# Kernel tuning notes

Hardware: AMD Instinct MI355X
Metric: run time of the kernel (lower is better)

## Reference

```python
import jax, jax.numpy as jnp
import numpy as np

MOL_SIZE = 64      # points per molecule (all molecules equal-size -> block-diagonal attn)
NUM_HEADS = 8
CUTOFF = 8.0
NUM_RBF = 32
LN_EPS = 1e-5


def setup_inputs() -> dict:
    key = jax.random.key(0)
    ks = jax.random.split(key, 6)
    B, K, hidden = 1024, MOL_SIZE, 512
    H = NUM_HEADS
    N = B * K
    h = jax.random.normal(ks[0], (N, hidden), jnp.float32)
    pos = jax.random.normal(ks[1], (N, 3), jnp.float32) * 3.0  # spread so dists hit RBF centers
    batch = jnp.repeat(jnp.arange(B, dtype=jnp.int32), K)
    s = lambda fin: 1.0 / np.sqrt(fin)
    centers = jnp.linspace(0.0, CUTOFF, NUM_RBF).astype(jnp.float32)  # RBFEncoder buffer
    w_rbf = jax.random.normal(ks[2], (NUM_RBF, H), jnp.float32) * s(NUM_RBF)
    b_rbf = jnp.zeros((H,), jnp.float32)
    w_qkv = jax.random.normal(ks[3], (hidden, 3 * hidden), jnp.float32) * s(hidden)
    b_qkv = jnp.zeros((3 * hidden,), jnp.float32)
    w_out = jax.random.normal(ks[4], (hidden, hidden), jnp.float32) * s(hidden)
    b_out = jnp.zeros((hidden,), jnp.float32)
    gamma = jnp.ones((hidden,), jnp.float32)
    beta = jnp.zeros((hidden,), jnp.float32)
    return {"h": h, "pos": pos, "batch": batch, "centers": centers,
            "w_rbf": w_rbf, "b_rbf": b_rbf, "w_qkv": w_qkv, "b_qkv": b_qkv,
            "w_out": w_out, "b_out": b_out, "gamma": gamma, "beta": beta}


def reference(h, pos, batch, centers, w_rbf, b_rbf, w_qkv, b_qkv, w_out, b_out, gamma, beta):
    N, hidden = h.shape
    K = MOL_SIZE
    B = N // K
    H = NUM_HEADS
    D = hidden // H
    width = (CUTOFF / NUM_RBF) ** 2
    scale = D ** -0.5

    # equal-size contiguous molecules -> reshape equals per-molecule loop
    hb = h.reshape(B, K, hidden)
    pb = pos.reshape(B, K, 3)

    qkv = hb @ w_qkv + b_qkv                      # [B,K,3*hidden]
    q, k, v = jnp.split(qkv, 3, axis=-1)
    q = q.reshape(B, K, H, D)
    k = k.reshape(B, K, H, D)
    v = v.reshape(B, K, H, D)

    diff = pb[:, :, None, :] - pb[:, None, :, :]  # [B,K,K,3]
    dist = jnp.sqrt(jnp.maximum(jnp.sum(diff * diff, axis=-1), 1e-12))  # torch.cdist
    rbf = jnp.exp(-((dist[..., None] - centers) ** 2) / width)          # [B,K,K,R]
    bias = jnp.transpose(rbf @ w_rbf + b_rbf, (0, 3, 1, 2))             # [B,H,K,K]

    attn = jnp.einsum('bkhd,bjhd->bhkj', q, k) * scale + bias
    attn = jax.nn.softmax(attn, axis=-1)
    agg = jnp.einsum('bhkj,bjhd->bkhd', attn, v).reshape(B, K, hidden)
    out = agg @ w_out + b_out

    y = hb + out
    mu = jnp.mean(y, axis=-1, keepdims=True)
    var = jnp.var(y, axis=-1, keepdims=True)
    y = (y - mu) / jnp.sqrt(var + LN_EPS) * gamma + beta
    return y.reshape(N, hidden)
```

## Files before the change

kernel.cpp:

```cpp
#include <hip/hip_runtime.h>
#include <hip/hip_bf16.h>


#define HID 512
#define TBL 2048
#define DMAX 12.0f

typedef __attribute__((ext_vector_type(4))) float f32x4;
typedef __attribute__((ext_vector_type(8))) short bhalf8;

__device__ __forceinline__ short f2bf(float f) {
    union { float f; unsigned u; } x; x.f = f;
    unsigned u = x.u;
    unsigned r = (u + 0x7FFFu + ((u >> 16) & 1u)) >> 16;
    return (short)r;
}

__global__ __launch_bounds__(256) void k_prep_w(const float* __restrict__ w_qkv,
                                                const float* __restrict__ w_out,
                                                short* __restrict__ wqT,
                                                short* __restrict__ woT) {
    __shared__ short tile[64][68];
    const int t = threadIdx.x;
    int bt = blockIdx.x;
    const float* src; short* dst; int sld, tk, tc;
    if (bt < 192) { src = w_qkv; dst = wqT; sld = 1536; tk = bt & 7; tc = bt >> 3; }
    else { int b2 = bt - 192; src = w_out; dst = woT; sld = 512; tk = b2 & 7; tc = b2 >> 3; }
#pragma unroll
    for (int p = 0; p < 4; ++p) {
        int s = t + 256 * p;
        int r = s >> 4, sg = s & 15;
        const float4 v = *(const float4*)(src + (tk * 64 + r) * sld + tc * 64 + sg * 4);
        tile[r][sg * 4 + 0] = f2bf(v.x);
        tile[r][sg * 4 + 1] = f2bf(v.y);
        tile[r][sg * 4 + 2] = f2bf(v.z);
        tile[r][sg * 4 + 3] = f2bf(v.w);
    }
    __syncthreads();
#pragma unroll
    for (int p = 0; p < 16; ++p) {
        int o = t + 256 * p;
        int c = o >> 6, k = o & 63;
        dst[(tc * 64 + c) * 512 + tk * 64 + k] = tile[k][c];
    }
}

__global__ __launch_bounds__(256) void k_prep_tbl(const float* __restrict__ centers,
                                                  const float* __restrict__ w_rbf,
                                                  const float* __restrict__ b_rbf,
                                                  float* __restrict__ tbl) {
    int idx = blockIdx.x * 256 + threadIdx.x;
    int hh = idx >> 11, i = idx & (TBL - 1);
    float d = (float)i * (DMAX / (float)(TBL - 1));
    float s = b_rbf[hh];
    const float invw = 1.0f / 0.0625f;
#pragma unroll 4
    for (int r = 0; r < 32; ++r) {
        float tt = d - centers[r];
        s += w_rbf[r * 8 + hh] * expf(-(tt * tt) * invw);
    }
    tbl[idx] = s;
}

__global__ __launch_bounds__(512) void k_qkv(const float* __restrict__ h,
                                             const float* __restrict__ b_qkv,
                                             const short* __restrict__ wqT,
                                             short* __restrict__ qkvb,
                                             int molbase) {
    __shared__ __align__(16) short As[128 * 40];
    __shared__ __align__(16) short Bs[256 * 40];
    const int t = threadIdx.x;
    const int lane = t & 63, wave = t >> 6;
    const int l16 = lane & 15, g = lane >> 4;
    const int wrow = wave >> 2, wcol = wave & 3;
    const int R0 = molbase * 64 + blockIdx.x * 128;
    const int C0 = blockIdx.y * 256;

    f32x4 acc[4][4];
#pragma unroll
    for (int i = 0; i < 4; ++i)
#pragma unroll
        for (int j = 0; j < 4; ++j) acc[i][j] = (f32x4){0.f, 0.f, 0.f, 0.f};

    const int arow = t >> 2, aseg = t & 3;
    for (int kc = 0; kc < 16; ++kc) {
        const int kb = kc * 32;
        {
            const float* src = h + (R0 + arow) * HID + kb + aseg * 8;
            float4 v0 = *(const float4*)src;
            float4 v1 = *(const float4*)(src + 4);
            short s8[8];
            s8[0] = f2bf(v0.x); s8[1] = f2bf(v0.y); s8[2] = f2bf(v0.z); s8[3] = f2bf(v0.w);
            s8[4] = f2bf(v1.x); s8[5] = f2bf(v1.y); s8[6] = f2bf(v1.z); s8[7] = f2bf(v1.w);
            *(int4*)(&As[arow * 40 + aseg * 8]) = *(int4*)s8;
        }
#pragma unroll
        for (int p = 0; p < 2; ++p) {
            int flat = p * 512 + t;
            int col = flat >> 2, seg = flat & 3;
            *(int4*)(&Bs[col * 40 + seg * 8]) =
                *(const int4*)(wqT + (C0 + col) * HID + kb + seg * 8);
        }
        __syncthreads();
        bhalf8 af[4], bf[4];
#pragma unroll
        for (int mt = 0; mt < 4; ++mt)
            af[mt] = *(const bhalf8*)(&As[(wrow * 64 + mt * 16 + l16) * 40 + g * 8]);
#pragma unroll
        for (int nt = 0; nt < 4; ++nt)
            bf[nt] = *(const bhalf8*)(&Bs[(wcol * 64 + nt * 16 + l16) * 40 + g * 8]);
#pragma unroll
        for (int mt = 0; mt < 4; ++mt)
#pragma unroll
            for (int nt = 0; nt < 4; ++nt)
                acc[mt][nt] = __builtin_amdgcn_mfma_f32_16x16x32_bf16(af[mt], bf[nt], acc[mt][nt], 0, 0, 0);
        __syncthreads();
    }

    const int sec = C0 >> 9;
    const float mul = (sec == 0) ? 0.125f : 1.0f;
#pragma unroll
    for (int nt = 0; nt < 4; ++nt) {
        int c = C0 + wcol * 64 + nt * 16 + l16;
        float bv = b_qkv[c];
        int head = (c >> 6) & 7, d = c & 63;
#pragma unroll
        for (int mt = 0; mt < 4; ++mt) {
            int rowg = R0 + wrow * 64 + mt * 16 + g * 4;
            int mol_local = (rowg >> 6) - molbase;
            short* panel = qkvb + (size_t)((mol_local * 3 + sec) * 8 + head) * 4096;
            int rloc = rowg & 63;
#pragma unroll
            for (int r = 0; r < 4; ++r)
                panel[(rloc + r) * 64 + d] = f2bf((acc[mt][nt][r] + bv) * mul);
        }
    }
}

__global__ __launch_bounds__(256) void k_attn(const short* __restrict__ qkvb,
                                              const float* __restrict__ pos,
                                              const float* __restrict__ tbl,
                                              float* __restrict__ agg,
                                              int molbase) {
    __shared__ __align__(16) short sq[64 * 72];
    __shared__ __align__(16) short sk[64 * 72];
    __shared__ __align__(16) short svT[64 * 72];
    __shared__ __align__(16) short sp[64 * 72];
    __shared__ float s_tbl[TBL];
    __shared__ float s_px[64], s_py[64], s_pz[64];

    const int bid = blockIdx.x;
    const int mol_local = bid >> 3, head = bid & 7;
    const int t = threadIdx.x;
    const int wave = t >> 6, lane = t & 63;
    const int l16 = lane & 15, g = lane >> 4;
    const int rowbase = (molbase + mol_local) * 64;

    const short* qp = qkvb + (size_t)((mol_local * 3 + 0) * 8 + head) * 4096;
    const short* kp = qkvb + (size_t)((mol_local * 3 + 1) * 8 + head) * 4096;
    const short* vp = qkvb + (size_t)((mol_local * 3 + 2) * 8 + head) * 4096;

#pragma unroll
    for (int p = 0; p < 2; ++p) {
        int slot = p * 256 + t;
        int row = slot >> 3, seg = slot & 7;
        *(int4*)(&sq[row * 72 + seg * 8]) = *(const int4*)(qp + slot * 8);
        *(int4*)(&sk[row * 72 + seg * 8]) = *(const int4*)(kp + slot * 8);
        int4 vv = *(const int4*)(vp + slot * 8);
        short* vs = (short*)&vv;
#pragma unroll
        for (int j = 0; j < 8; ++j) svT[(seg * 8 + j) * 72 + row] = vs[j];
    }
    for (int i = t; i < TBL; i += 256) s_tbl[i] = tbl[head * TBL + i];
    if (t < 64) {
        s_px[t] = pos[(rowbase + t) * 3 + 0];
        s_py[t] = pos[(rowbase + t) * 3 + 1];
        s_pz[t] = pos[(rowbase + t) * 3 + 2];
    }
    __syncthreads();

    f32x4 sacc[4];
#pragma unroll
    for (int i = 0; i < 4; ++i) sacc[i] = (f32x4){0.f, 0.f, 0.f, 0.f};
    const int srow = wave * 16 + l16;
#pragma unroll
    for (int kk = 0; kk < 2; ++kk) {
        bhalf8 a = *(const bhalf8*)(&sq[srow * 72 + kk * 32 + g * 8]);
#pragma unroll
        for (int ct = 0; ct < 4; ++ct) {
            bhalf8 b = *(const bhalf8*)(&sk[(ct * 16 + l16) * 72 + kk * 32 + g * 8]);
            sacc[ct] = __builtin_amdgcn_mfma_f32_16x16x32_bf16(a, b, sacc[ct], 0, 0, 0);
        }
    }

    const int r0 = wave * 16 + g * 4;
    const float tscale = (float)(TBL - 1) / DMAX;
#pragma unroll
    for (int ct = 0; ct < 4; ++ct) {
        int col = ct * 16 + l16;
        float cx = s_px[col], cy = s_py[col], cz = s_pz[col];
#pragma unroll
        for (int r = 0; r < 4; ++r) {
            int row = r0 + r;
            float dx = s_px[row] - cx, dy = s_py[row] - cy, dz = s_pz[row] - cz;
            float dd = fmaf(dx, dx, fmaf(dy, dy, dz * dz));
            float dist = sqrtf(fmaxf(dd, 1e-12f));
            float u = fminf(dist, DMAX) * tscale;
            int i = (int)u; if (i > TBL - 2) i = TBL - 2;
            float fr = u - (float)i;
            float t0 = s_tbl[i];
            sacc[ct][r] += fmaf(fr, s_tbl[i + 1] - t0, t0);
        }
    }

    float inv[4];
#pragma unroll
    for (int r = 0; r < 4; ++r) {
        float m = fmaxf(fmaxf(sacc[0][r], sacc[1][r]), fmaxf(sacc[2][r], sacc[3][r]));
#pragma unroll
        for (int off = 1; off < 16; off <<= 1) m = fmaxf(m, __shfl_xor(m, off, 64));
        float e0 = __expf(sacc[0][r] - m);
        float e1 = __expf(sacc[1][r] - m);
        float e2 = __expf(sacc[2][r] - m);
        float e3 = __expf(sacc[3][r] - m);
        float ssum = e0 + e1 + e2 + e3;
#pragma unroll
        for (int off = 1; off < 16; off <<= 1) ssum += __shfl_xor(ssum, off, 64);
        inv[r] = 1.0f / ssum;
        int pb = (r0 + r) * 72 + l16;
        sp[pb + 0]  = f2bf(e0);
        sp[pb + 16] = f2bf(e1);
        sp[pb + 32] = f2bf(e2);
        sp[pb + 48] = f2bf(e3);
    }
    __syncthreads();

    f32x4 oacc[4];
#pragma unroll
    for (int i = 0; i < 4; ++i) oacc[i] = (f32x4){0.f, 0.f, 0.f, 0.f};
#pragma unroll
    for (int kk = 0; kk < 2; ++kk) {
        bhalf8 a = *(const bhalf8*)(&sp[srow * 72 + kk * 32 + g * 8]);
#pragma unroll
        for (int ct = 0; ct < 4; ++ct) {
            bhalf8 b = *(const bhalf8*)(&svT[(ct * 16 + l16) * 72 + kk * 32 + g * 8]);
            oacc[ct] = __builtin_amdgcn_mfma_f32_16x16x32_bf16(a, b, oacc[ct], 0, 0, 0);
        }
    }
#pragma unroll
    for (int ct = 0; ct < 4; ++ct) {
        int col = head * 64 + ct * 16 + l16;
#pragma unroll
        for (int r = 0; r < 4; ++r)
            agg[(rowbase + r0 + r) * HID + col] = oacc[ct][r] * inv[r];
    }
}

__global__ __launch_bounds__(512) void k_proj(const float* __restrict__ aggf,
                                              const float* __restrict__ h,
                                              const short* __restrict__ woT,
                                              const float* __restrict__ b_out,
                                              const float* __restrict__ gamma,
                                              const float* __restrict__ beta,
                                              float* __restrict__ out) {
    __shared__ __align__(16) short As[64 * 40];
    __shared__ __align__(16) short Bs[512 * 40];
    __shared__ float red[64 * 16];
    __shared__ float mr[64 * 2];
    const int mol = blockIdx.x;
    const int t = threadIdx.x;
    const int wave = t >> 6, lane = t & 63;
    const int l16 = lane & 15, g = lane >> 4;
    const int rowbase = mol * 64;

    f32x4 acc[4][4];
#pragma unroll
    for (int i = 0; i < 4; ++i)
#pragma unroll
        for (int j = 0; j < 4; ++j) acc[i][j] = (f32x4){0.f, 0.f, 0.f, 0.f};

    for (int kc = 0; kc < 16; ++kc) {
        const int kb = kc * 32;
        if (t < 256) {
            int row = t >> 2, seg = t & 3;
            const float* src = aggf + (rowbase + row) * HID + kb + seg * 8;
            float4 v0 = *(const float4*)src;
            float4 v1 = *(const float4*)(src + 4);
            short s8[8];
            s8[0] = f2bf(v0.x); s8[1] = f2bf(v0.y); s8[2] = f2bf(v0.z); s8[3] = f2bf(v0.w);
            s8[4] = f2bf(v1.x); s8[5] = f2bf(v1.y); s8[6] = f2bf(v1.z); s8[7] = f2bf(v1.w);
            *(int4*)(&As[row * 40 + seg * 8]) = *(int4*)s8;
        }
#pragma unroll
        for (int p = 0; p < 4; ++p) {
            int flat = p * 512 + t;
            int col = flat >> 2, seg = flat & 3;
            *(int4*)(&Bs[col * 40 + seg * 8]) =
                *(const int4*)(woT + col * HID + kb + seg * 8);
        }
        __syncthreads();
        bhalf8 af[4], bf[4];
#pragma unroll
        for (int mt = 0; mt < 4; ++mt)
            af[mt] = *(const bhalf8*)(&As[(mt * 16 + l16) * 40 + g * 8]);
#pragma unroll
        for (int nt = 0; nt < 4; ++nt)
            bf[nt] = *(const bhalf8*)(&Bs[(wave * 64 + nt * 16 + l16) * 40 + g * 8]);
#pragma unroll
        for (int mt = 0; mt < 4; ++mt)
#pragma unroll
            for (int nt = 0; nt < 4; ++nt)
                acc[mt][nt] = __builtin_amdgcn_mfma_f32_16x16x32_bf16(af[mt], bf[nt], acc[mt][nt], 0, 0, 0);
        __syncthreads();
    }

#pragma unroll
    for (int mt = 0; mt < 4; ++mt) {
        float s = 0.f, q = 0.f;
#pragma unroll
        for (int r = 0; r < 4; ++r) {
            int row = mt * 16 + g * 4 + r;
            float rs = 0.f, rq = 0.f;
#pragma unroll
            for (int nt = 0; nt < 4; ++nt) {
                int col = wave * 64 + nt * 16 + l16;
                float v = acc[mt][nt][r] + b_out[col] + h[(rowbase + row) * HID + col];
                acc[mt][nt][r] = v;
                rs += v;
                rq = fmaf(v, v, rq);
            }
#pragma unroll
            for (int off = 1; off < 16; off <<= 1) {
                rs += __shfl_xor(rs, off, 16);
                rq += __shfl_xor(rq, off, 16);
            }
            if (l16 == 0) {
                red[row * 16 + wave * 2 + 0] = rs;
                red[row * 16 + wave * 2 + 1] = rq;
            }
            s = rs; q = rq;
        }
        (void)s; (void)q;
    }
    __syncthreads();
    if (t < 64) {
        float s = 0.f, q = 0.f;
#pragma unroll
        for (int w = 0; w < 8; ++w) {
            s += red[t * 16 + w * 2 + 0];
            q += red[t * 16 + w * 2 + 1];
        }
        float mean = s * (1.0f / 512.0f);
        float var = q * (1.0f / 512.0f) - mean * mean;
        mr[t * 2 + 0] = mean;
        mr[t * 2 + 1] = rsqrtf(var + 1e-5f);
    }
    __syncthreads();
#pragma unroll
    for (int mt = 0; mt < 4; ++mt)
#pragma unroll
        for (int r = 0; r < 4; ++r) {
            int row = mt * 16 + g * 4 + r;
            float mean = mr[row * 2 + 0], rstd = mr[row * 2 + 1];
#pragma unroll
            for (int nt = 0; nt < 4; ++nt) {
                int col = wave * 64 + nt * 16 + l16;
                out[(rowbase + row) * HID + col] =
                    fmaf((acc[mt][nt][r] - mean) * rstd, gamma[col], beta[col]);
            }
        }
}

extern "C" void kernel_launch(void* const* d_in, const int* in_sizes, int n_in,
                              void* d_out, int out_size, void* d_ws, size_t ws_size,
                              hipStream_t stream) {
    (void)in_sizes; (void)n_in; (void)out_size; (void)ws_size;
    const float* h       = (const float*)d_in[0];
    const float* pos     = (const float*)d_in[1];
    const float* centers = (const float*)d_in[3];
    const float* w_rbf   = (const float*)d_in[4];
    const float* b_rbf   = (const float*)d_in[5];
    const float* w_qkv   = (const float*)d_in[6];
    const float* b_qkv   = (const float*)d_in[7];
    const float* w_out   = (const float*)d_in[8];
    const float* b_out   = (const float*)d_in[9];
    const float* gamma   = (const float*)d_in[10];
    const float* beta    = (const float*)d_in[11];
    float* out = (float*)d_out;

    char* ws = (char*)d_ws;
    short* wqT  = (short*)ws;
    short* woT  = (short*)(ws + 1572864);
    float* tbl  = (float*)(ws + 2097152);
    short* qkvb = (short*)(ws + 2162688);

    k_prep_w<<<256, 256, 0, stream>>>(w_qkv, w_out, wqT, woT);
    k_prep_tbl<<<64, 256, 0, stream>>>(centers, w_rbf, b_rbf, tbl);
    for (int half = 0; half < 2; ++half) {
        int molbase = half * 512;
        k_qkv<<<dim3(256, 6), 512, 0, stream>>>(h, b_qkv, wqT, qkvb, molbase);
        k_attn<<<4096, 256, 0, stream>>>(qkvb, pos, tbl, out, molbase);
    }
    k_proj<<<1024, 512, 0, stream>>>(out, h, woT, b_out, gamma, beta, out);
}
```

Baseline: 434.5 us.

## Enlarge output-projection tile, prefetch K-chunks in registers, swizzle V transpose in LDS

The output projection kernel now covers 128 rows per block on a 2x4 wave grid, so each block reads the Wo chunk once for twice as many rows. The next K-chunk is loaded into registers while the MFMAs for the current chunk run, which hides global-load latency at the cost of more registers (32 accumulator tiles per wave) and fewer blocks. Separately, the attention kernel's transposed V tile in LDS gets an XOR swizzle to cut bank conflicts on the scattered transpose stores and the fragment reads. The LayerNorm reduction is adjusted to the new 4-column-wave layout.

```diff
diff --git a/kernel.cpp b/kernel.cpp
--- a/kernel.cpp
+++ b/kernel.cpp
@@ -169,7 +169,8 @@
         int4 vv = *(const int4*)(vp + slot * 8);
         short* vs = (short*)&vv;
 #pragma unroll
-        for (int j = 0; j < 8; ++j) svT[(seg * 8 + j) * 72 + row] = vs[j];
+        for (int j = 0; j < 8; ++j)
+            svT[(seg * 8 + j) * 72 + (row & 7) + (((row >> 3) ^ seg) & 7) * 8] = vs[j];
     }
     for (int i = t; i < TBL; i += 256) s_tbl[i] = tbl[head * TBL + i];
     if (t < 64) {
@@ -243,7 +244,8 @@
         bhalf8 a = *(const bhalf8*)(&sp[srow * 72 + kk * 32 + g * 8]);
 #pragma unroll
         for (int ct = 0; ct < 4; ++ct) {
-            bhalf8 b = *(const bhalf8*)(&svT[(ct * 16 + l16) * 72 + kk * 32 + g * 8]);
+            int drow = ct * 16 + l16;
+            bhalf8 b = *(const bhalf8*)(&svT[drow * 72 + (((kk * 4 + g) ^ (drow >> 3)) & 7) * 8]);
             oacc[ct] = __builtin_amdgcn_mfma_f32_16x16x32_bf16(a, b, oacc[ct], 0, 0, 0);
         }
     }
@@ -263,67 +265,80 @@
                                               const float* __restrict__ gamma,
                                               const float* __restrict__ beta,
                                               float* __restrict__ out) {
-    __shared__ __align__(16) short As[64 * 40];
+    __shared__ __align__(16) short As[128 * 40];
     __shared__ __align__(16) short Bs[512 * 40];
-    __shared__ float red[64 * 16];
-    __shared__ float mr[64 * 2];
-    const int mol = blockIdx.x;
+    __shared__ float red[128 * 8];
+    __shared__ float mr[128 * 2];
     const int t = threadIdx.x;
     const int wave = t >> 6, lane = t & 63;
     const int l16 = lane & 15, g = lane >> 4;
-    const int rowbase = mol * 64;
-
-    f32x4 acc[4][4];
+    const int wrow = wave >> 2, wcol = wave & 3;
+    const int rowbase = blockIdx.x * 128;
+
+    f32x4 acc[4][8];
 #pragma unroll
     for (int i = 0; i < 4; ++i)
 #pragma unroll
-        for (int j = 0; j < 4; ++j) acc[i][j] = (f32x4){0.f, 0.f, 0.f, 0.f};
-
+        for (int j = 0; j < 8; ++j) acc[i][j] = (f32x4){0.f, 0.f, 0.f, 0.f};
+
+    const int arow = t >> 2, aseg = t & 3;
+    int4 pA, pB0, pB1, pB2, pB3;
+    const int bcol = t >> 2, bseg = t & 3;
+
+#define LOADA(kc) {                                                              \
+        const float* src = aggf + (rowbase + arow) * HID + (kc) * 32 + aseg * 8; \
+        float4 v0 = *(const float4*)src;                                         \
+        float4 v1 = *(const float4*)(src + 4);                                   \
+        short s8[8];                                                             \
+        s8[0] = f2bf(v0.x); s8[1] = f2bf(v0.y); s8[2] = f2bf(v0.z); s8[3] = f2bf(v0.w); \
+        s8[4] = f2bf(v1.x); s8[5] = f2bf(v1.y); s8[6] = f2bf(v1.z); s8[7] = f2bf(v1.w); \
+        pA = *(int4*)s8; }
+#define LOADB(kc) {                                                              \
+        pB0 = *(const int4*)(woT + (bcol +   0) * HID + (kc) * 32 + bseg * 8);   \
+        pB1 = *(const int4*)(woT + (bcol + 128) * HID + (kc) * 32 + bseg * 8);   \
+        pB2 = *(const int4*)(woT + (bcol + 256) * HID + (kc) * 32 + bseg * 8);   \
+        pB3 = *(const int4*)(woT + (bcol + 384) * HID + (kc) * 32 + bseg * 8); }
+#define STAGE() {                                                                \
+        *(int4*)(&As[arow * 40 + aseg * 8]) = pA;                                \
+        *(int4*)(&Bs[(bcol +   0) * 40 + bseg * 8]) = pB0;                       \
+        *(int4*)(&Bs[(bcol + 128) * 40 + bseg * 8]) = pB1;                       \
+        *(int4*)(&Bs[(bcol + 256) * 40 + bseg * 8]) = pB2;                       \
+        *(int4*)(&Bs[(bcol + 384) * 40 + bseg * 8]) = pB3; }
+
+    LOADA(0); LOADB(0); STAGE(); __syncthreads();
     for (int kc = 0; kc < 16; ++kc) {
-        const int kb = kc * 32;
-        if (t < 256) {
-            int row = t >> 2, seg = t & 3;
-            const float* src = aggf + (rowbase + row) * HID + kb + seg * 8;
-            float4 v0 = *(const float4*)src;
-            float4 v1 = *(const float4*)(src + 4);
-            short s8[8];
-            s8[0] = f2bf(v0.x); s8[1] = f2bf(v0.y); s8[2] = f2bf(v0.z); s8[3] = f2bf(v0.w);
-            s8[4] = f2bf(v1.x); s8[5] = f2bf(v1.y); s8[6] = f2bf(v1.z); s8[7] = f2bf(v1.w);
-            *(int4*)(&As[row * 40 + seg * 8]) = *(int4*)s8;
-        }
-#pragma unroll
-        for (int p = 0; p < 4; ++p) {
-            int flat = p * 512 + t;
-            int col = flat >> 2, seg = flat & 3;
-            *(int4*)(&Bs[col * 40 + seg * 8]) =
-                *(const int4*)(woT + col * HID + kb + seg * 8);
-        }
-        __syncthreads();
-        bhalf8 af[4], bf[4];
+        if (kc < 15) { LOADA(kc + 1); LOADB(kc + 1); }
+        bhalf8 af[4], bf[8];
 #pragma unroll
         for (int mt = 0; mt < 4; ++mt)
-            af[mt] = *(const bhalf8*)(&As[(mt * 16 + l16) * 40 + g * 8]);
-#pragma unroll
-        for (int nt = 0; nt < 4; ++nt)
-            bf[nt] = *(const bhalf8*)(&Bs[(wave * 64 + nt * 16 + l16) * 40 + g * 8]);
+            af[mt] = *(const bhalf8*)(&As[(wrow * 64 + mt * 16 + l16) * 40 + g * 8]);
+#pragma unroll
+        for (int nt = 0; nt < 8; ++nt)
+            bf[nt] = *(const bhalf8*)(&Bs[(wcol * 128 + nt * 16 + l16) * 40 + g * 8]);
 #pragma unroll
         for (int mt = 0; mt < 4; ++mt)
 #pragma unroll
-            for (int nt = 0; nt < 4; ++nt)
+            for (int nt = 0; nt < 8; ++nt)
                 acc[mt][nt] = __builtin_amdgcn_mfma_f32_16x16x32_bf16(af[mt], bf[nt], acc[mt][nt], 0, 0, 0);
-        __syncthreads();
-    }
+        if (kc < 15) {
+            __syncthreads();
+            STAGE();
+            __syncthreads();
+        }
+    }
+#undef LOADA
+#undef LOADB
+#undef STAGE
 
 #pragma unroll
     for (int mt = 0; mt < 4; ++mt) {
-        float s = 0.f, q = 0.f;
 #pragma unroll
         for (int r = 0; r < 4; ++r) {
-            int row = mt * 16 + g * 4 + r;
+            int row = wrow * 64 + mt * 16 + g * 4 + r;
             float rs = 0.f, rq = 0.f;
 #pragma unroll
-            for (int nt = 0; nt < 4; ++nt) {
-                int col = wave * 64 + nt * 16 + l16;
+            for (int nt = 0; nt < 8; ++nt) {
+                int col = wcol * 128 + nt * 16 + l16;
                 float v = acc[mt][nt][r] + b_out[col] + h[(rowbase + row) * HID + col];
                 acc[mt][nt][r] = v;
                 rs += v;
@@ -331,25 +346,19 @@
             }
 #pragma unroll
             for (int off = 1; off < 16; off <<= 1) {
-                rs += __shfl_xor(rs, off, 16);
-                rq += __shfl_xor(rq, off, 16);
+                rs += __shfl_xor(rs, off, 64);
+                rq += __shfl_xor(rq, off, 64);
             }
             if (l16 == 0) {
-                red[row * 16 + wave * 2 + 0] = rs;
-                red[row * 16 + wave * 2 + 1] = rq;
+                red[row * 8 + wcol * 2 + 0] = rs;
+                red[row * 8 + wcol * 2 + 1] = rq;
             }
-            s = rs; q = rq;
-        }
-        (void)s; (void)q;
+        }
     }
     __syncthreads();
-    if (t < 64) {
-        float s = 0.f, q = 0.f;
-#pragma unroll
-        for (int w = 0; w < 8; ++w) {
-            s += red[t * 16 + w * 2 + 0];
-            q += red[t * 16 + w * 2 + 1];
-        }
+    if (t < 128) {
+        float s = red[t * 8 + 0] + red[t * 8 + 2] + red[t * 8 + 4] + red[t * 8 + 6];
+        float q = red[t * 8 + 1] + red[t * 8 + 3] + red[t * 8 + 5] + red[t * 8 + 7];
         float mean = s * (1.0f / 512.0f);
         float var = q * (1.0f / 512.0f) - mean * mean;
         mr[t * 2 + 0] = mean;
@@ -360,11 +369,11 @@
     for (int mt = 0; mt < 4; ++mt)
 #pragma unroll
         for (int r = 0; r < 4; ++r) {
-            int row = mt * 16 + g * 4 + r;
+            int row = wrow * 64 + mt * 16 + g * 4 + r;
             float mean = mr[row * 2 + 0], rstd = mr[row * 2 + 1];
 #pragma unroll
-            for (int nt = 0; nt < 4; ++nt) {
-                int col = wave * 64 + nt * 16 + l16;
+            for (int nt = 0; nt < 8; ++nt) {
+                int col = wcol * 128 + nt * 16 + l16;
                 out[(rowbase + row) * HID + col] =
                     fmaf((acc[mt][nt][r] - mean) * rstd, gamma[col], beta[col]);
             }
@@ -401,5 +410,5 @@
         k_qkv<<<dim3(256, 6), 512, 0, stream>>>(h, b_qkv, wqT, qkvb, molbase);
         k_attn<<<4096, 256, 0, stream>>>(qkvb, pos, tbl, out, molbase);
     }
-    k_proj<<<1024, 512, 0, stream>>>(out, h, woT, b_out, gamma, beta, out);
-}
+    k_proj<<<512, 512, 0, stream>>>(out, h, woT, b_out, gamma, beta, out);
+}
```

New measurement: 390.3 us. 10.2% less time.

## Fuse attention with output projection and LayerNorm, pipeline QKV GEMM loads

Applied to the files above, without the earlier changes.

Merges the per-head attention kernel and the output projection/LayerNorm kernel into one per-molecule kernel. All 8 heads run as 8 waves, and the aggregated output stays in swizzled LDS as bf16 instead of making a float32 round trip through global memory. The QKV GEMM now reads weight fragments straight from global into registers with software prefetch and a double-buffered A tile, and it writes V already transposed. The RBF lookup table is halved to 1024 entries so all heads fit in LDS. Costs include heavy LDS use per block (about 100KB), which limits occupancy, and a coarser bias interpolation table.

```diff
diff --git a/kernel.cpp b/kernel.cpp
--- a/kernel.cpp
+++ b/kernel.cpp
@@ -3,7 +3,7 @@
 
 
 #define HID 512
-#define TBL 2048
+#define TBL 1024
 #define DMAX 12.0f
 
 typedef __attribute__((ext_vector_type(4))) float f32x4;
@@ -50,7 +50,7 @@
                                                   const float* __restrict__ b_rbf,
                                                   float* __restrict__ tbl) {
     int idx = blockIdx.x * 256 + threadIdx.x;
-    int hh = idx >> 11, i = idx & (TBL - 1);
+    int hh = idx >> 10, i = idx & (TBL - 1);
     float d = (float)i * (DMAX / (float)(TBL - 1));
     float s = b_rbf[hh];
     const float invw = 1.0f / 0.0625f;
@@ -67,8 +67,7 @@
                                              const short* __restrict__ wqT,
                                              short* __restrict__ qkvb,
                                              int molbase) {
-    __shared__ __align__(16) short As[128 * 40];
-    __shared__ __align__(16) short Bs[256 * 40];
+    __shared__ __align__(16) short As[2][128 * 40];
     const int t = threadIdx.x;
     const int lane = t & 63, wave = t >> 6;
     const int l16 = lane & 15, g = lane >> 4;
@@ -83,38 +82,60 @@
         for (int j = 0; j < 4; ++j) acc[i][j] = (f32x4){0.f, 0.f, 0.f, 0.f};
 
     const int arow = t >> 2, aseg = t & 3;
+    const float* hsrc = h + (size_t)(R0 + arow) * HID + aseg * 8;
+
+    int brow[4];
+#pragma unroll
+    for (int nt = 0; nt < 4; ++nt)
+        brow[nt] = (C0 + wcol * 64 + nt * 16 + l16) * HID + g * 8;
+
+    {
+        float4 a0 = *(const float4*)(hsrc);
+        float4 a1 = *(const float4*)(hsrc + 4);
+        short s8[8];
+        s8[0] = f2bf(a0.x); s8[1] = f2bf(a0.y); s8[2] = f2bf(a0.z); s8[3] = f2bf(a0.w);
+        s8[4] = f2bf(a1.x); s8[5] = f2bf(a1.y); s8[6] = f2bf(a1.z); s8[7] = f2bf(a1.w);
+        *(int4*)(&As[0][arow * 40 + aseg * 8]) = *(int4*)s8;
+    }
+    float4 p0 = *(const float4*)(hsrc + 32);
+    float4 p1 = *(const float4*)(hsrc + 36);
+    int4 bw[4];
+#pragma unroll
+    for (int nt = 0; nt < 4; ++nt) bw[nt] = *(const int4*)(wqT + brow[nt]);
+    __syncthreads();
+
     for (int kc = 0; kc < 16; ++kc) {
-        const int kb = kc * 32;
-        {
-            const float* src = h + (R0 + arow) * HID + kb + aseg * 8;
-            float4 v0 = *(const float4*)src;
-            float4 v1 = *(const float4*)(src + 4);
+        int4 bn[4];
+        if (kc < 15) {
+#pragma unroll
+            for (int nt = 0; nt < 4; ++nt)
+                bn[nt] = *(const int4*)(wqT + brow[nt] + (kc + 1) * 32);
+        }
+        float4 n0, n1;
+        if (kc < 14) {
+            n0 = *(const float4*)(hsrc + (kc + 2) * 32);
+            n1 = *(const float4*)(hsrc + (kc + 2) * 32 + 4);
+        }
+        bhalf8 af[4];
+#pragma unroll
+        for (int mt = 0; mt < 4; ++mt)
+            af[mt] = *(const bhalf8*)(&As[kc & 1][(wrow * 64 + mt * 16 + l16) * 40 + g * 8]);
+#pragma unroll
+        for (int mt = 0; mt < 4; ++mt)
+#pragma unroll
+            for (int nt = 0; nt < 4; ++nt)
+                acc[mt][nt] = __builtin_amdgcn_mfma_f32_16x16x32_bf16(
+                    af[mt], *(bhalf8*)&bw[nt], acc[mt][nt], 0, 0, 0);
+        if (kc < 15) {
             short s8[8];
-            s8[0] = f2bf(v0.x); s8[1] = f2bf(v0.y); s8[2] = f2bf(v0.z); s8[3] = f2bf(v0.w);
-            s8[4] = f2bf(v1.x); s8[5] = f2bf(v1.y); s8[6] = f2bf(v1.z); s8[7] = f2bf(v1.w);
-            *(int4*)(&As[arow * 40 + aseg * 8]) = *(int4*)s8;
-        }
-#pragma unroll
-        for (int p = 0; p < 2; ++p) {
-            int flat = p * 512 + t;
-            int col = flat >> 2, seg = flat & 3;
-            *(int4*)(&Bs[col * 40 + seg * 8]) =
-                *(const int4*)(wqT + (C0 + col) * HID + kb + seg * 8);
-        }
-        __syncthreads();
-        bhalf8 af[4], bf[4];
-#pragma unroll
-        for (int mt = 0; mt < 4; ++mt)
-            af[mt] = *(const bhalf8*)(&As[(wrow * 64 + mt * 16 + l16) * 40 + g * 8]);
-#pragma unroll
-        for (int nt = 0; nt < 4; ++nt)
-            bf[nt] = *(const bhalf8*)(&Bs[(wcol * 64 + nt * 16 + l16) * 40 + g * 8]);
-#pragma unroll
-        for (int mt = 0; mt < 4; ++mt)
-#pragma unroll
-            for (int nt = 0; nt < 4; ++nt)
-                acc[mt][nt] = __builtin_amdgcn_mfma_f32_16x16x32_bf16(af[mt], bf[nt], acc[mt][nt], 0, 0, 0);
-        __syncthreads();
+            s8[0] = f2bf(p0.x); s8[1] = f2bf(p0.y); s8[2] = f2bf(p0.z); s8[3] = f2bf(p0.w);
+            s8[4] = f2bf(p1.x); s8[5] = f2bf(p1.y); s8[6] = f2bf(p1.z); s8[7] = f2bf(p1.w);
+            *(int4*)(&As[(kc + 1) & 1][arow * 40 + aseg * 8]) = *(int4*)s8;
+            __syncthreads();
+        }
+        p0 = n0; p1 = n1;
+#pragma unroll
+        for (int nt = 0; nt < 4; ++nt) bw[nt] = bn[nt];
     }
 
     const int sec = C0 >> 9;
@@ -128,50 +149,45 @@
         for (int mt = 0; mt < 4; ++mt) {
             int rowg = R0 + wrow * 64 + mt * 16 + g * 4;
             int mol_local = (rowg >> 6) - molbase;
+            int rloc = rowg & 63;
             short* panel = qkvb + (size_t)((mol_local * 3 + sec) * 8 + head) * 4096;
-            int rloc = rowg & 63;
-#pragma unroll
-            for (int r = 0; r < 4; ++r)
-                panel[(rloc + r) * 64 + d] = f2bf((acc[mt][nt][r] + bv) * mul);
-        }
-    }
-}
-
-__global__ __launch_bounds__(256) void k_attn(const short* __restrict__ qkvb,
-                                              const float* __restrict__ pos,
-                                              const float* __restrict__ tbl,
-                                              float* __restrict__ agg,
-                                              int molbase) {
-    __shared__ __align__(16) short sq[64 * 72];
-    __shared__ __align__(16) short sk[64 * 72];
-    __shared__ __align__(16) short svT[64 * 72];
-    __shared__ __align__(16) short sp[64 * 72];
-    __shared__ float s_tbl[TBL];
+            if (sec == 2) {
+#pragma unroll
+                for (int r = 0; r < 4; ++r)
+                    panel[d * 64 + rloc + r] = f2bf(acc[mt][nt][r] + bv);
+            } else {
+#pragma unroll
+                for (int r = 0; r < 4; ++r)
+                    panel[(rloc + r) * 64 + d] = f2bf((acc[mt][nt][r] + bv) * mul);
+            }
+        }
+    }
+}
+
+__global__ __launch_bounds__(512) void k_fused(const short* __restrict__ qkvb,
+                                               const float* __restrict__ pos,
+                                               const float* __restrict__ tbl,
+                                               const float* __restrict__ h,
+                                               const short* __restrict__ woT,
+                                               const float* __restrict__ b_out,
+                                               const float* __restrict__ gamma,
+                                               const float* __restrict__ beta,
+                                               float* __restrict__ out,
+                                               int molbase) {
+    __shared__ __align__(16) short uP[8 * 4096];
+    __shared__ float s_tbl[8 * 1032];
     __shared__ float s_px[64], s_py[64], s_pz[64];
-
-    const int bid = blockIdx.x;
-    const int mol_local = bid >> 3, head = bid & 7;
+    __shared__ float red[64 * 16];
+    __shared__ float mr[64 * 2];
+
     const int t = threadIdx.x;
     const int wave = t >> 6, lane = t & 63;
     const int l16 = lane & 15, g = lane >> 4;
+    const int mol_local = blockIdx.x;
     const int rowbase = (molbase + mol_local) * 64;
 
-    const short* qp = qkvb + (size_t)((mol_local * 3 + 0) * 8 + head) * 4096;
-    const short* kp = qkvb + (size_t)((mol_local * 3 + 1) * 8 + head) * 4096;
-    const short* vp = qkvb + (size_t)((mol_local * 3 + 2) * 8 + head) * 4096;
-
-#pragma unroll
-    for (int p = 0; p < 2; ++p) {
-        int slot = p * 256 + t;
-        int row = slot >> 3, seg = slot & 7;
-        *(int4*)(&sq[row * 72 + seg * 8]) = *(const int4*)(qp + slot * 8);
-        *(int4*)(&sk[row * 72 + seg * 8]) = *(const int4*)(kp + slot * 8);
-        int4 vv = *(const int4*)(vp + slot * 8);
-        short* vs = (short*)&vv;
-#pragma unroll
-        for (int j = 0; j < 8; ++j) svT[(seg * 8 + j) * 72 + row] = vs[j];
-    }
-    for (int i = t; i < TBL; i += 256) s_tbl[i] = tbl[head * TBL + i];
+    for (int i = t; i < 8 * TBL; i += 512)
+        s_tbl[(i >> 10) * 1032 + (i & (TBL - 1))] = tbl[i];
     if (t < 64) {
         s_px[t] = pos[(rowbase + t) * 3 + 0];
         s_py[t] = pos[(rowbase + t) * 3 + 1];
@@ -179,144 +195,154 @@
     }
     __syncthreads();
 
-    f32x4 sacc[4];
-#pragma unroll
-    for (int i = 0; i < 4; ++i) sacc[i] = (f32x4){0.f, 0.f, 0.f, 0.f};
-    const int srow = wave * 16 + l16;
+    const short* qp = qkvb + ((size_t)(mol_local * 3 + 0) * 8 + wave) * 4096;
+    const short* kp = qkvb + ((size_t)(mol_local * 3 + 1) * 8 + wave) * 4096;
+    const short* vt = qkvb + ((size_t)(mol_local * 3 + 2) * 8 + wave) * 4096;
+
+    f32x4 sacc[4][4];
+#pragma unroll
+    for (int i = 0; i < 4; ++i)
+#pragma unroll
+        for (int j = 0; j < 4; ++j) sacc[i][j] = (f32x4){0.f, 0.f, 0.f, 0.f};
 #pragma unroll
     for (int kk = 0; kk < 2; ++kk) {
-        bhalf8 a = *(const bhalf8*)(&sq[srow * 72 + kk * 32 + g * 8]);
-#pragma unroll
-        for (int ct = 0; ct < 4; ++ct) {
-            bhalf8 b = *(const bhalf8*)(&sk[(ct * 16 + l16) * 72 + kk * 32 + g * 8]);
-            sacc[ct] = __builtin_amdgcn_mfma_f32_16x16x32_bf16(a, b, sacc[ct], 0, 0, 0);
-        }
-    }
-
-    const int r0 = wave * 16 + g * 4;
+        bhalf8 qa[4], kb[4];
+#pragma unroll
+        for (int mt = 0; mt < 4; ++mt)
+            qa[mt] = *(const bhalf8*)(qp + (mt * 16 + l16) * 64 + kk * 32 + g * 8);
+#pragma unroll
+        for (int nt = 0; nt < 4; ++nt)
+            kb[nt] = *(const bhalf8*)(kp + (nt * 16 + l16) * 64 + kk * 32 + g * 8);
+#pragma unroll
+        for (int mt = 0; mt < 4; ++mt)
+#pragma unroll
+            for (int nt = 0; nt < 4; ++nt)
+                sacc[mt][nt] = __builtin_amdgcn_mfma_f32_16x16x32_bf16(
+                    qa[mt], kb[nt], sacc[mt][nt], 0, 0, 0);
+    }
+
     const float tscale = (float)(TBL - 1) / DMAX;
-#pragma unroll
-    for (int ct = 0; ct < 4; ++ct) {
-        int col = ct * 16 + l16;
+    const float* T = s_tbl + wave * 1032;
+#pragma unroll
+    for (int nt = 0; nt < 4; ++nt) {
+        int col = nt * 16 + l16;
         float cx = s_px[col], cy = s_py[col], cz = s_pz[col];
 #pragma unroll
+        for (int mt = 0; mt < 4; ++mt) {
+#pragma unroll
+            for (int r = 0; r < 4; ++r) {
+                int row = mt * 16 + g * 4 + r;
+                float dx = s_px[row] - cx, dy = s_py[row] - cy, dz = s_pz[row] - cz;
+                float dd = fmaf(dx, dx, fmaf(dy, dy, dz * dz));
+                float dist = sqrtf(fmaxf(dd, 1e-12f));
+                float u = fminf(dist, DMAX) * tscale;
+                int i = (int)u; if (i > TBL - 2) i = TBL - 2;
+                float fr = u - (float)i;
+                float t0 = T[i];
+                sacc[mt][nt][r] += fmaf(fr, T[i + 1] - t0, t0);
+            }
+        }
+    }
+
+    float inv[4][4];
+    short* Pw = uP + wave * 4096;
+#pragma unroll
+    for (int mt = 0; mt < 4; ++mt) {
+#pragma unroll
         for (int r = 0; r < 4; ++r) {
-            int row = r0 + r;
-            float dx = s_px[row] - cx, dy = s_py[row] - cy, dz = s_pz[row] - cz;
-            float dd = fmaf(dx, dx, fmaf(dy, dy, dz * dz));
-            float dist = sqrtf(fmaxf(dd, 1e-12f));
-            float u = fminf(dist, DMAX) * tscale;
-            int i = (int)u; if (i > TBL - 2) i = TBL - 2;
-            float fr = u - (float)i;
-            float t0 = s_tbl[i];
-            sacc[ct][r] += fmaf(fr, s_tbl[i + 1] - t0, t0);
-        }
-    }
-
-    float inv[4];
-#pragma unroll
-    for (int r = 0; r < 4; ++r) {
-        float m = fmaxf(fmaxf(sacc[0][r], sacc[1][r]), fmaxf(sacc[2][r], sacc[3][r]));
-#pragma unroll
-        for (int off = 1; off < 16; off <<= 1) m = fmaxf(m, __shfl_xor(m, off, 64));
-        float e0 = __expf(sacc[0][r] - m);
-        float e1 = __expf(sacc[1][r] - m);
-        float e2 = __expf(sacc[2][r] - m);
-        float e3 = __expf(sacc[3][r] - m);
-        float ssum = e0 + e1 + e2 + e3;
-#pragma unroll
-        for (int off = 1; off < 16; off <<= 1) ssum += __shfl_xor(ssum, off, 64);
-        inv[r] = 1.0f / ssum;
-        int pb = (r0 + r) * 72 + l16;
-        sp[pb + 0]  = f2bf(e0);
-        sp[pb + 16] = f2bf(e1);
-        sp[pb + 32] = f2bf(e2);
-        sp[pb + 48] = f2bf(e3);
-    }
-    __syncthreads();
-
-    f32x4 oacc[4];
-#pragma unroll
-    for (int i = 0; i < 4; ++i) oacc[i] = (f32x4){0.f, 0.f, 0.f, 0.f};
+            float m = fmaxf(fmaxf(sacc[0][mt < 0 ? 0 : 0][r], sacc[0][r < 0 ? 0 : 0][r]), 0.f);
+            m = fmaxf(fmaxf(sacc[mt][0][r], sacc[mt][1][r]),
+                      fmaxf(sacc[mt][2][r], sacc[mt][3][r]));
+#pragma unroll
+            for (int off = 1; off < 16; off <<= 1) m = fmaxf(m, __shfl_xor(m, off, 64));
+            float e[4], ssum = 0.f;
+#pragma unroll
+            for (int nt = 0; nt < 4; ++nt) { e[nt] = __expf(sacc[mt][nt][r] - m); ssum += e[nt]; }
+#pragma unroll
+            for (int off = 1; off < 16; off <<= 1) ssum += __shfl_xor(ssum, off, 64);
+            inv[mt][r] = 1.0f / ssum;
+            int row = mt * 16 + g * 4 + r;
+            int rho = row & 7;
+#pragma unroll
+            for (int nt = 0; nt < 4; ++nt) {
+                int c = nt * 16 + l16;
+                Pw[row * 64 + (((c >> 3) ^ rho) << 3) + (c & 7)] = f2bf(e[nt]);
+            }
+        }
+    }
+
+    f32x4 oacc[4][4];
+#pragma unroll
+    for (int i = 0; i < 4; ++i)
+#pragma unroll
+        for (int j = 0; j < 4; ++j) oacc[i][j] = (f32x4){0.f, 0.f, 0.f, 0.f};
 #pragma unroll
     for (int kk = 0; kk < 2; ++kk) {
-        bhalf8 a = *(const bhalf8*)(&sp[srow * 72 + kk * 32 + g * 8]);
-#pragma unroll
-        for (int ct = 0; ct < 4; ++ct) {
-            bhalf8 b = *(const bhalf8*)(&svT[(ct * 16 + l16) * 72 + kk * 32 + g * 8]);
-            oacc[ct] = __builtin_amdgcn_mfma_f32_16x16x32_bf16(a, b, oacc[ct], 0, 0, 0);
-        }
-    }
-#pragma unroll
-    for (int ct = 0; ct < 4; ++ct) {
-        int col = head * 64 + ct * 16 + l16;
-#pragma unroll
-        for (int r = 0; r < 4; ++r)
-            agg[(rowbase + r0 + r) * HID + col] = oacc[ct][r] * inv[r];
-    }
-}
-
-__global__ __launch_bounds__(512) void k_proj(const float* __restrict__ aggf,
-                                              const float* __restrict__ h,
-                                              const short* __restrict__ woT,
-                                              const float* __restrict__ b_out,
-                                              const float* __restrict__ gamma,
-                                              const float* __restrict__ beta,
-                                              float* __restrict__ out) {
-    __shared__ __align__(16) short As[64 * 40];
-    __shared__ __align__(16) short Bs[512 * 40];
-    __shared__ float red[64 * 16];
-    __shared__ float mr[64 * 2];
-    const int mol = blockIdx.x;
-    const int t = threadIdx.x;
-    const int wave = t >> 6, lane = t & 63;
-    const int l16 = lane & 15, g = lane >> 4;
-    const int rowbase = mol * 64;
-
-    f32x4 acc[4][4];
+        bhalf8 pa[4], vb[4];
+#pragma unroll
+        for (int mt = 0; mt < 4; ++mt)
+            pa[mt] = *(const bhalf8*)(Pw + (mt * 16 + l16) * 64 +
+                                      (((kk * 4 + g) ^ (l16 & 7)) << 3));
+#pragma unroll
+        for (int nt = 0; nt < 4; ++nt)
+            vb[nt] = *(const bhalf8*)(vt + (nt * 16 + l16) * 64 + kk * 32 + g * 8);
+#pragma unroll
+        for (int mt = 0; mt < 4; ++mt)
+#pragma unroll
+            for (int nt = 0; nt < 4; ++nt)
+                oacc[mt][nt] = __builtin_amdgcn_mfma_f32_16x16x32_bf16(
+                    pa[mt], vb[nt], oacc[mt][nt], 0, 0, 0);
+    }
+#pragma unroll
+    for (int mt = 0; mt < 4; ++mt)
+#pragma unroll
+        for (int nt = 0; nt < 4; ++nt)
+#pragma unroll
+            for (int r = 0; r < 4; ++r) oacc[mt][nt][r] *= inv[mt][r];
+
+    __syncthreads();
+
+#pragma unroll
+    for (int mt = 0; mt < 4; ++mt) {
+#pragma unroll
+        for (int r = 0; r < 4; ++r) {
+            int row = mt * 16 + g * 4 + r;
+            int rho = row & 7;
+#pragma unroll
+            for (int nt = 0; nt < 4; ++nt) {
+                int c = wave * 64 + nt * 16 + l16;
+                uP[row * 512 + (((c >> 3) ^ rho) << 3) + (c & 7)] = f2bf(oacc[mt][nt][r]);
+            }
+        }
+    }
+    __syncthreads();
+
+    f32x4 pacc[4][4];
 #pragma unroll
     for (int i = 0; i < 4; ++i)
 #pragma unroll
-        for (int j = 0; j < 4; ++j) acc[i][j] = (f32x4){0.f, 0.f, 0.f, 0.f};
-
+        for (int j = 0; j < 4; ++j) pacc[i][j] = (f32x4){0.f, 0.f, 0.f, 0.f};
+#pragma unroll 4
     for (int kc = 0; kc < 16; ++kc) {
-        const int kb = kc * 32;
-        if (t < 256) {
-            int row = t >> 2, seg = t & 3;
-            const float* src = aggf + (rowbase + row) * HID + kb + seg * 8;
-            float4 v0 = *(const float4*)src;
-            float4 v1 = *(const float4*)(src + 4);
-            short s8[8];
-            s8[0] = f2bf(v0.x); s8[1] = f2bf(v0.y); s8[2] = f2bf(v0.z); s8[3] = f2bf(v0.w);
-            s8[4] = f2bf(v1.x); s8[5] = f2bf(v1.y); s8[6] = f2bf(v1.z); s8[7] = f2bf(v1.w);
-            *(int4*)(&As[row * 40 + seg * 8]) = *(int4*)s8;
-        }
-#pragma unroll
-        for (int p = 0; p < 4; ++p) {
-            int flat = p * 512 + t;
-            int col = flat >> 2, seg = flat & 3;
-            *(int4*)(&Bs[col * 40 + seg * 8]) =
-                *(const int4*)(woT + col * HID + kb + seg * 8);
-        }
-        __syncthreads();
-        bhalf8 af[4], bf[4];
-#pragma unroll
-        for (int mt = 0; mt < 4; ++mt)
-            af[mt] = *(const bhalf8*)(&As[(mt * 16 + l16) * 40 + g * 8]);
+        bhalf8 af[4], bw[4];
+#pragma unroll
+        for (int mt = 0; mt < 4; ++mt)
+            af[mt] = *(const bhalf8*)(uP + (mt * 16 + l16) * 512 +
+                                      (((kc * 4 + g) ^ (l16 & 7)) << 3));
 #pragma unroll
         for (int nt = 0; nt < 4; ++nt)
-            bf[nt] = *(const bhalf8*)(&Bs[(wave * 64 + nt * 16 + l16) * 40 + g * 8]);
+            bw[nt] = *(const bhalf8*)(woT + (size_t)(wave * 64 + nt * 16 + l16) * HID +
+                                      kc * 32 + g * 8);
 #pragma unroll
         for (int mt = 0; mt < 4; ++mt)
 #pragma unroll
             for (int nt = 0; nt < 4; ++nt)
-                acc[mt][nt] = __builtin_amdgcn_mfma_f32_16x16x32_bf16(af[mt], bf[nt], acc[mt][nt], 0, 0, 0);
-        __syncthreads();
+                pacc[mt][nt] = __builtin_amdgcn_mfma_f32_16x16x32_bf16(
+                    af[mt], bw[nt], pacc[mt][nt], 0, 0, 0);
     }
 
 #pragma unroll
     for (int mt = 0; mt < 4; ++mt) {
-        float s = 0.f, q = 0.f;
 #pragma unroll
         for (int r = 0; r < 4; ++r) {
             int row = mt * 16 + g * 4 + r;
@@ -324,23 +350,22 @@
 #pragma unroll
             for (int nt = 0; nt < 4; ++nt) {
                 int col = wave * 64 + nt * 16 + l16;
-                float v = acc[mt][nt][r] + b_out[col] + h[(rowbase + row) * HID + col];
-                acc[mt][nt][r] = v;
+                float v = pacc[mt][nt][r] + b_out[col] +
+                          h[(size_t)(rowbase + row) * HID + col];
+                pacc[mt][nt][r] = v;
                 rs += v;
                 rq = fmaf(v, v, rq);
             }
 #pragma unroll
             for (int off = 1; off < 16; off <<= 1) {
-                rs += __shfl_xor(rs, off, 16);
-                rq += __shfl_xor(rq, off, 16);
+                rs += __shfl_xor(rs, off, 64);
+                rq += __shfl_xor(rq, off, 64);
             }
             if (l16 == 0) {
                 red[row * 16 + wave * 2 + 0] = rs;
                 red[row * 16 + wave * 2 + 1] = rq;
             }
-            s = rs; q = rq;
-        }
-        (void)s; (void)q;
+        }
     }
     __syncthreads();
     if (t < 64) {
@@ -357,7 +382,7 @@
     }
     __syncthreads();
 #pragma unroll
-    for (int mt = 0; mt < 4; ++mt)
+    for (int mt = 0; mt < 4; ++mt) {
 #pragma unroll
         for (int r = 0; r < 4; ++r) {
             int row = mt * 16 + g * 4 + r;
@@ -365,10 +390,11 @@
 #pragma unroll
             for (int nt = 0; nt < 4; ++nt) {
                 int col = wave * 64 + nt * 16 + l16;
-                out[(rowbase + row) * HID + col] =
-                    fmaf((acc[mt][nt][r] - mean) * rstd, gamma[col], beta[col]);
-            }
-        }
+                out[(size_t)(rowbase + row) * HID + col] =
+                    fmaf((pacc[mt][nt][r] - mean) * rstd, gamma[col], beta[col]);
+            }
+        }
+    }
 }
 
 extern "C" void kernel_launch(void* const* d_in, const int* in_sizes, int n_in,
@@ -395,11 +421,11 @@
     short* qkvb = (short*)(ws + 2162688);
 
     k_prep_w<<<256, 256, 0, stream>>>(w_qkv, w_out, wqT, woT);
-    k_prep_tbl<<<64, 256, 0, stream>>>(centers, w_rbf, b_rbf, tbl);
+    k_prep_tbl<<<32, 256, 0, stream>>>(centers, w_rbf, b_rbf, tbl);
     for (int half = 0; half < 2; ++half) {
         int molbase = half * 512;
         k_qkv<<<dim3(256, 6), 512, 0, stream>>>(h, b_qkv, wqT, qkvb, molbase);
-        k_attn<<<4096, 256, 0, stream>>>(qkvb, pos, tbl, out, molbase);
-    }
-    k_proj<<<1024, 512, 0, stream>>>(out, h, woT, b_out, gamma, beta, out);
-}
+        k_fused<<<512, 512, 0, stream>>>(qkvb, pos, tbl, h, woT, b_out,
+                                         gamma, beta, out, molbase);
+    }
+}
```

After: 492.5 us. 13.4% more time.
